# Optimization experiments

Measured on AMD Instinct MI355X. Metric: run time of the kernel, lower is better.

## Reference

```python
import jax, jax.numpy as jnp
import numpy as np

D_MODEL = 1024
N_HEADS = 16
D_HEAD = D_MODEL // N_HEADS
BATCH = 2
SEQ = 2048


def setup_inputs() -> dict:
    key = jax.random.key(0)
    ks = jax.random.split(key, 16)
    s = 0.02
    d = D_MODEL
    return {
        "x": jax.random.normal(ks[0], (BATCH, SEQ, d), jnp.float32),
        "Wq": jax.random.normal(ks[1], (d, d), jnp.float32) * s,
        "bq": jnp.zeros((d,), jnp.float32),
        "Wk": jax.random.normal(ks[2], (d, d), jnp.float32) * s,
        "bk": jnp.zeros((d,), jnp.float32),
        "Wv": jax.random.normal(ks[3], (d, d), jnp.float32) * s,
        "bv": jnp.zeros((d,), jnp.float32),
        "Wo": jax.random.normal(ks[4], (d, d), jnp.float32) * s,
        "bo": jnp.zeros((d,), jnp.float32),
        "Wt": jax.random.normal(ks[5], (d, 1), jnp.float32) * s,
        "bt": jnp.zeros((1,), jnp.float32),
        "Wg": jax.random.normal(ks[6], (d, d), jnp.float32) * s,
        "bg": jnp.zeros((d,), jnp.float32),
    }


def _evolved_attention(x, Wq, bq, Wk, bk, Wv, bv, Wo, bo, Wt, bt, Wg, bg):
    B, S, D = x.shape
    H, dh = N_HEADS, D_HEAD

    def heads(y):  # [B,S,D] -> [B,H,S,dh]
        return y.reshape(B, S, H, dh).transpose(0, 2, 1, 3)

    q = heads(x @ Wq + bq)
    k = heads(x @ Wk + bk)
    v = heads(x @ Wv + bv)

    # cosine similarity (F.normalize with eps=1e-12)
    qn = q / jnp.maximum(jnp.linalg.norm(q, axis=-1, keepdims=True), 1e-12)
    kn = k / jnp.maximum(jnp.linalg.norm(k, axis=-1, keepdims=True), 1e-12)
    scores = jnp.einsum("bhqd,bhkd->bhqk", qn, kn)

    # adaptive temperature: sigmoid(temp_proj(mean_s x)) + 0.5, shape [B,1]
    temp = jax.nn.sigmoid(x.mean(axis=1) @ Wt + bt) + 0.5  # [B,1]
    scores = scores / temp[:, None, None, :]  # broadcast [B,1,1,1]

    # sparsemax-style: softmax over top-k (k = S//4), scattered back
    kk = max(1, S // 4)
    vals, idx = jax.lax.top_k(scores, kk)          # [B,H,S,kk]
    w = jax.nn.softmax(vals, axis=-1)
    rows = jnp.arange(B * H * S)[:, None]
    attn = (
        jnp.zeros((B * H * S, S), scores.dtype)
        .at[rows, idx.reshape(-1, kk)]
        .set(w.reshape(-1, kk))
        .reshape(B, H, S, S)
    )

    out = jnp.einsum("bhqk,bhkd->bhqd", attn, v)
    out = out.transpose(0, 2, 1, 3).reshape(B, S, D)
    out = out @ Wo + bo

    # highway gating
    gate = jax.nn.sigmoid(x @ Wg + bg)
    return gate * out + (1.0 - gate) * x


def reference(x, Wq, bq, Wk, bk, Wv, bv, Wo, bo, Wt, bt, Wg, bg):
    return _evolved_attention(x, Wq, bq, Wk, bk, Wv, bv, Wo, bo, Wt, bt, Wg, bg)
```

## Files before the change

### kernel.cpp

```cpp
#include <hip/hip_runtime.h>

typedef unsigned short u16;
typedef __attribute__((ext_vector_type(4))) float f32x4;
typedef __attribute__((ext_vector_type(8))) short bf16x8;
typedef __attribute__((ext_vector_type(4))) int i32x4;

#define BB 2
#define SS 2048
#define DD 1024
#define HH 16
#define DH 64
#define KK 512

#define OFF_SCAL  ((size_t)0)
#define OFF_WT    ((size_t)256)
#define OFF_XB    (OFF_WT + (size_t)5*1024*1024*2)
#define OFF_AO    OFF_XB
#define OFF_QH    (OFF_XB + (size_t)4096*1024*2)
#define OFF_QN    (OFF_QH + (size_t)4096*4096*2)
#define OFF_KN    (OFF_QN + (size_t)4096*1024*2)
#define OFF_VT    (OFF_KN + (size_t)4096*1024*2)

__device__ __forceinline__ float b2f(u16 u) { return __uint_as_float(((unsigned)u) << 16); }
__device__ __forceinline__ u16 f2b(float f) {
    unsigned u = __float_as_uint(f);
    return (u16)((u + 0x7fffu + ((u >> 16) & 1u)) >> 16);
}

__global__ __launch_bounds__(256) void convert_x(const float* x, u16* xb) {
    int i = (blockIdx.x * 256 + threadIdx.x) * 4;
    float4 v = *(const float4*)(x + i);
    u16 r0 = f2b(v.x), r1 = f2b(v.y), r2 = f2b(v.z), r3 = f2b(v.w);
    xb[i] = r0; xb[i + 1] = r1; xb[i + 2] = r2; xb[i + 3] = r3;
}

__global__ __launch_bounds__(256) void transpose_w(
        const float* Wq, const float* Wk, const float* Wv, const float* Wg, const float* Wo,
        u16* WT) {
    int z = blockIdx.z;
    const float* src = (z == 0) ? Wq : (z == 1) ? Wk : (z == 2) ? Wv : (z == 3) ? Wg : Wo;
    u16* dst = WT + (size_t)z * 1024 * 1024;
    __shared__ float tile[64][65];
    int n0 = blockIdx.x * 64, k0 = blockIdx.y * 64;
    int rbase = threadIdx.x >> 6, c = threadIdx.x & 63;
#pragma unroll
    for (int i = 0; i < 16; i++) {
        int r = i * 4 + rbase;
        tile[r][c] = src[(size_t)(k0 + r) * 1024 + n0 + c];
    }
    __syncthreads();
#pragma unroll
    for (int i = 0; i < 16; i++) {
        int r = i * 4 + rbase;
        dst[(size_t)(n0 + r) * 1024 + k0 + c] = f2b(tile[c][r]);
    }
}

__global__ __launch_bounds__(256) void temp_partial(const float* x, const float* Wt,
                                                    float* accbuf) {
    int b = blockIdx.x >> 5, ch = blockIdx.x & 31;
    float a = 0.f;
    for (int si = 0; si < 64; si++) {
        int s = ch * 64 + si;
        const float* xr = x + ((size_t)(b * SS + s)) * DD;
#pragma unroll
        for (int k = 0; k < 4; k++) {
            int c = threadIdx.x + k * 256;
            a += xr[c] * Wt[c];
        }
    }
    for (int o = 32; o; o >>= 1) a += __shfl_xor(a, o);
    __shared__ float red[4];
    if ((threadIdx.x & 63) == 0) red[threadIdx.x >> 6] = a;
    __syncthreads();
    if (threadIdx.x == 0) atomicAdd(&accbuf[b], red[0] + red[1] + red[2] + red[3]);
}

__global__ void temp_final(const float* accbuf, const float* bt, float* itemp) {
    int t = threadIdx.x;
    if (t < BB) {
        float v = accbuf[t] / (float)SS + bt[0];
        float tmp = 1.f / (1.f + __expf(-v)) + 0.5f;
        itemp[t] = 1.f / tmp;
    }
}

__global__ __launch_bounds__(256) void gemm_qkvg(
        const u16* X, const u16* WT,
        const float* bq, const float* bk, const float* bv, const float* bg, u16* Qh) {
    __shared__ u16 la[64 * 40];
    __shared__ u16 lb[64 * 40];
    int tid = threadIdx.x, wid = tid >> 6, lane = tid & 63;
    int m0 = blockIdx.x * 64, n0 = blockIdx.y * 64;
    int quad = lane >> 4, ml = lane & 15;
    f32x4 acc[4];
#pragma unroll
    for (int i = 0; i < 4; i++) acc[i] = (f32x4){0.f, 0.f, 0.f, 0.f};

    int sr = tid >> 2, sg = tid & 3;
    for (int k0 = 0; k0 < 1024; k0 += 32) {
        __syncthreads();
        *(i32x4*)&la[sr * 40 + sg * 8] = *(const i32x4*)&X[(size_t)(m0 + sr) * 1024 + k0 + sg * 8];
        *(i32x4*)&lb[sr * 40 + sg * 8] = *(const i32x4*)&WT[(size_t)(n0 + sr) * 1024 + k0 + sg * 8];
        __syncthreads();
        bf16x8 a = *(const bf16x8*)&la[(wid * 16 + ml) * 40 + quad * 8];
#pragma unroll
        for (int nt = 0; nt < 4; nt++) {
            bf16x8 bfr = *(const bf16x8*)&lb[(nt * 16 + ml) * 40 + quad * 8];
            acc[nt] = __builtin_amdgcn_mfma_f32_16x16x32_bf16(a, bfr, acc[nt], 0, 0, 0);
        }
    }
#pragma unroll
    for (int nt = 0; nt < 4; nt++) {
        int col = n0 + nt * 16 + ml;
        int mat = col >> 10, bc = col & 1023;
        const float* bp = (mat == 0) ? bq : (mat == 1) ? bk : (mat == 2) ? bv : bg;
        float bias = bp[bc];
#pragma unroll
        for (int r = 0; r < 4; r++) {
            int row = m0 + wid * 16 + quad * 4 + r;
            Qh[(size_t)row * 4096 + col] = f2b(acc[nt][r] + bias);
        }
    }
}

__global__ __launch_bounds__(256) void norm_repack(const u16* Qh, u16* qn, u16* kn, u16* vt) {
    int wid = threadIdx.x >> 6, lane = threadIdx.x & 63;
    int idx = blockIdx.x * 4 + wid;
    int token = idx >> 4, h = idx & 15;
    int b = token >> 11, s = token & 2047;
    int bh = b * HH + h;
    const u16* rowp = Qh + (size_t)token * 4096 + h * 64;
    float q = b2f(rowp[lane]);
    float k = b2f(rowp[1024 + lane]);
    u16 v = rowp[2048 + lane];
    float sq = q * q, sk = k * k;
    for (int o = 32; o; o >>= 1) { sq += __shfl_xor(sq, o); sk += __shfl_xor(sk, o); }
    float qd = fmaxf(sqrtf(sq), 1e-12f), kd = fmaxf(sqrtf(sk), 1e-12f);
    qn[((size_t)bh * SS + s) * DH + lane] = f2b(q / qd);
    kn[((size_t)bh * SS + s) * DH + lane] = f2b(k / kd);
    vt[((size_t)bh * DH + lane) * SS + s] = v;
}

#define EST 2088

__global__ __launch_bounds__(1024, 8) void attn_kernel(
        const u16* qn, const u16* kn, const u16* vt, const float* itemp, u16* ao) {
    __shared__ __align__(16) u16 e16[16 * EST];
    __shared__ float pvp[3][16][66];
    __shared__ float zrow_s[16];

    int tid = threadIdx.x, wid = tid >> 6, lane = tid & 63;
    int quad = lane >> 4, nl = lane & 15;
    int bh = blockIdx.x >> 7, qt = blockIdx.x & 127;
    int b = bh >> 4, h = bh & 15;
    const u16* qbase = qn + ((size_t)bh * SS + qt * 16) * DH;
    const u16* kbase = kn + (size_t)bh * SS * DH;
    const u16* vbase = vt + (size_t)bh * DH * SS;
    float it = itemp[b];

    bf16x8 aq0 = *(const bf16x8*)(qbase + nl * DH + quad * 8);
    bf16x8 aq1 = *(const bf16x8*)(qbase + nl * DH + 32 + quad * 8);

#pragma unroll 4
    for (int c = 0; c < 8; c++) {
        int j = c * 256 + wid * 16 + nl;
        const u16* kr = kbase + (size_t)j * DH;
        bf16x8 b0 = *(const bf16x8*)(kr + quad * 8);
        bf16x8 b1 = *(const bf16x8*)(kr + 32 + quad * 8);
        f32x4 acc = (f32x4){0.f, 0.f, 0.f, 0.f};
        acc = __builtin_amdgcn_mfma_f32_16x16x32_bf16(aq0, b0, acc, 0, 0, 0);
        acc = __builtin_amdgcn_mfma_f32_16x16x32_bf16(aq1, b1, acc, 0, 0, 0);
#pragma unroll
        for (int r = 0; r < 4; r++) e16[(quad * 4 + r) * EST + j] = f2b(acc[r] * it);
    }
    __syncthreads();

    {
        int row = wid;
        int key[32];
#pragma unroll
        for (int c = 0; c < 32; c++) {
            int raw = (int)e16[row * EST + c * 64 + lane];
            key[c] = (raw & 0x8000) ? (raw ^ 0xFFFF) : (raw | 0x8000);
        }
        int P = 0;
        for (int bit = 15; bit >= 0; bit--) {
            int cand = P | (1 << bit);
            int cnt = 0;
#pragma unroll
            for (int c = 0; c < 32; c++)
                cnt += (int)__popcll(__ballot(key[c] >= cand));
            if (cnt >= KK) P = cand;
        }
        float z = 0.f;
#pragma unroll
        for (int c = 0; c < 32; c++) {
            float e = 0.f;
            if (key[c] >= P) {
                int raw = (key[c] & 0x8000) ? (key[c] ^ 0x8000) : (key[c] ^ 0xFFFF);
                e = __expf(b2f((u16)raw));
            }
            z += e;
            e16[row * EST + c * 64 + lane] = f2b(e);
        }
#pragma unroll
        for (int o = 32; o; o >>= 1) z += __shfl_xor(z, o);
        if (lane == 0) zrow_s[row] = z;
    }
    __syncthreads();

    f32x4 accp = (f32x4){0.f, 0.f, 0.f, 0.f};
    int kq = wid >> 2, g = wid & 3;
    int dh = g * 16 + nl;
    const u16* vrow = vbase + (size_t)dh * SS;
#pragma unroll 4
    for (int c = 0; c < 8; c++) {
        int j0 = kq * 512 + c * 64;
#pragma unroll
        for (int ks = 0; ks < 2; ks++) {
            bf16x8 a = *(const bf16x8*)&e16[nl * EST + j0 + ks * 32 + quad * 8];
            bf16x8 bfr = *(const bf16x8*)(vrow + j0 + ks * 32 + quad * 8);
            accp = __builtin_amdgcn_mfma_f32_16x16x32_bf16(a, bfr, accp, 0, 0, 0);
        }
    }
    if (kq) {
#pragma unroll
        for (int r = 0; r < 4; r++) pvp[kq - 1][quad * 4 + r][dh] = accp[r];
    }
    __syncthreads();
    if (kq == 0) {
#pragma unroll
        for (int r = 0; r < 4; r++) {
            int q = quad * 4 + r;
            float val = (accp[r] + pvp[0][q][dh] + pvp[1][q][dh] + pvp[2][q][dh]) / zrow_s[q];
            size_t row = (size_t)(b * SS + qt * 16 + q);
            ao[row * DD + h * 64 + dh] = f2b(val);
        }
    }
}

__global__ __launch_bounds__(256) void gemm_out(
        const u16* AO, const u16* WTo, const float* bo,
        const u16* Qh, const float* x, float* out) {
    __shared__ u16 la[64 * 40];
    __shared__ u16 lb[64 * 40];
    int tid = threadIdx.x, wid = tid >> 6, lane = tid & 63;
    int m0 = blockIdx.x * 64, n0 = blockIdx.y * 64;
    int quad = lane >> 4, ml = lane & 15;
    f32x4 acc[4];
#pragma unroll
    for (int i = 0; i < 4; i++) acc[i] = (f32x4){0.f, 0.f, 0.f, 0.f};

    int sr = tid >> 2, sg = tid & 3;
    for (int k0 = 0; k0 < 1024; k0 += 32) {
        __syncthreads();
        *(i32x4*)&la[sr * 40 + sg * 8] = *(const i32x4*)&AO[(size_t)(m0 + sr) * 1024 + k0 + sg * 8];
        *(i32x4*)&lb[sr * 40 + sg * 8] = *(const i32x4*)&WTo[(size_t)(n0 + sr) * 1024 + k0 + sg * 8];
        __syncthreads();
        bf16x8 a = *(const bf16x8*)&la[(wid * 16 + ml) * 40 + quad * 8];
#pragma unroll
        for (int nt = 0; nt < 4; nt++) {
            bf16x8 bfr = *(const bf16x8*)&lb[(nt * 16 + ml) * 40 + quad * 8];
            acc[nt] = __builtin_amdgcn_mfma_f32_16x16x32_bf16(a, bfr, acc[nt], 0, 0, 0);
        }
    }
#pragma unroll
    for (int nt = 0; nt < 4; nt++) {
        int col = n0 + nt * 16 + ml;
        float bias = bo[col];
#pragma unroll
        for (int r = 0; r < 4; r++) {
            int row = m0 + wid * 16 + quad * 4 + r;
            float g = b2f(Qh[(size_t)row * 4096 + 3072 + col]);
            float gate = 1.f / (1.f + __expf(-g));
            float xv = x[(size_t)row * 1024 + col];
            float o = acc[nt][r] + bias;
            out[(size_t)row * 1024 + col] = gate * o + (1.f - gate) * xv;
        }
    }
}

extern "C" void kernel_launch(void* const* d_in, const int* in_sizes, int n_in,
                              void* d_out, int out_size, void* d_ws, size_t ws_size,
                              hipStream_t stream) {
    const float* x  = (const float*)d_in[0];
    const float* Wq = (const float*)d_in[1];
    const float* bq = (const float*)d_in[2];
    const float* Wk = (const float*)d_in[3];
    const float* bk = (const float*)d_in[4];
    const float* Wv = (const float*)d_in[5];
    const float* bv = (const float*)d_in[6];
    const float* Wo = (const float*)d_in[7];
    const float* bo = (const float*)d_in[8];
    const float* Wt = (const float*)d_in[9];
    const float* bt = (const float*)d_in[10];
    const float* Wg = (const float*)d_in[11];
    const float* bg = (const float*)d_in[12];

    char* w = (char*)d_ws;
    float* accbuf = (float*)(w + OFF_SCAL);
    float* itemp  = accbuf + 2;
    u16*   WT     = (u16*)(w + OFF_WT);
    u16*   xb     = (u16*)(w + OFF_XB);
    u16*   ao     = (u16*)(w + OFF_AO);
    u16*   Qh     = (u16*)(w + OFF_QH);
    u16*   qn     = (u16*)(w + OFF_QN);
    u16*   kn     = (u16*)(w + OFF_KN);
    u16*   vt     = (u16*)(w + OFF_VT);

    hipMemsetAsync(accbuf, 0, 2 * sizeof(float), stream);

    convert_x<<<4096, 256, 0, stream>>>(x, xb);
    transpose_w<<<dim3(16, 16, 5), 256, 0, stream>>>(Wq, Wk, Wv, Wg, Wo, WT);
    temp_partial<<<64, 256, 0, stream>>>(x, Wt, accbuf);
    temp_final<<<1, 64, 0, stream>>>(accbuf, bt, itemp);
    gemm_qkvg<<<dim3(64, 64), 256, 0, stream>>>(xb, WT, bq, bk, bv, bg, Qh);
    norm_repack<<<16384, 256, 0, stream>>>(Qh, qn, kn, vt);
    attn_kernel<<<4096, 1024, 0, stream>>>(qn, kn, vt, itemp, ao);
    gemm_out<<<dim3(64, 16), 256, 0, stream>>>(ao, WT + (size_t)4 * 1024 * 1024, bo, Qh, x,
                                               (float*)d_out);
}
```

Baseline: 548.1 us.

## Enlarge GEMM tiles with direct-to-LDS loads and vectorize top-k threshold search

Result: faster. 510.6 us (-6.8%).

```diff
diff --git a/kernel.cpp b/kernel.cpp
--- a/kernel.cpp
+++ b/kernel.cpp
@@ -25,6 +25,12 @@
 __device__ __forceinline__ u16 f2b(float f) {
     unsigned u = __float_as_uint(f);
     return (u16)((u + 0x7fffu + ((u >> 16) & 1u)) >> 16);
+}
+
+__device__ __forceinline__ void gload16(const u16* g, u16* l) {
+    __builtin_amdgcn_global_load_lds(
+        (__attribute__((address_space(1))) void*)g,
+        (__attribute__((address_space(3))) void*)l, 16, 0, 0);
 }
 
 __global__ __launch_bounds__(256) void convert_x(const float* x, u16* xb) {
@@ -88,40 +94,64 @@
 __global__ __launch_bounds__(256) void gemm_qkvg(
         const u16* X, const u16* WT,
         const float* bq, const float* bk, const float* bv, const float* bg, u16* Qh) {
-    __shared__ u16 la[64 * 40];
-    __shared__ u16 lb[64 * 40];
+    __shared__ __align__(16) u16 la[128 * 32];
+    __shared__ __align__(16) u16 lb[128 * 32];
     int tid = threadIdx.x, wid = tid >> 6, lane = tid & 63;
-    int m0 = blockIdx.x * 64, n0 = blockIdx.y * 64;
     int quad = lane >> 4, ml = lane & 15;
-    f32x4 acc[4];
-#pragma unroll
-    for (int i = 0; i < 4; i++) acc[i] = (f32x4){0.f, 0.f, 0.f, 0.f};
-
-    int sr = tid >> 2, sg = tid & 3;
+    int m0 = blockIdx.x * 128, n0 = blockIdx.y * 128;
+    int wr = wid >> 1, wc = wid & 1;
+
+    f32x4 acc[4][4];
+#pragma unroll
+    for (int i = 0; i < 4; i++)
+#pragma unroll
+        for (int j = 0; j < 4; j++) acc[i][j] = (f32x4){0.f, 0.f, 0.f, 0.f};
+
+    int t0 = wid * 2, t1 = t0 + 1;
+    int r0 = lane >> 2, kp = lane & 3;
+    const u16* ga0 = X + (size_t)(m0 + t0 * 16 + r0) * 1024 + kp * 8;
+    const u16* ga1 = X + (size_t)(m0 + t1 * 16 + r0) * 1024 + kp * 8;
+    const u16* gb0 = WT + (size_t)(n0 + t0 * 16 + r0) * 1024 + kp * 8;
+    const u16* gb1 = WT + (size_t)(n0 + t1 * 16 + r0) * 1024 + kp * 8;
+    u16* la0 = la + t0 * 512; u16* la1 = la + t1 * 512;
+    u16* lb0 = lb + t0 * 512; u16* lb1 = lb + t1 * 512;
+
     for (int k0 = 0; k0 < 1024; k0 += 32) {
+        gload16(ga0 + k0, la0);
+        gload16(ga1 + k0, la1);
+        gload16(gb0 + k0, lb0);
+        gload16(gb1 + k0, lb1);
         __syncthreads();
-        *(i32x4*)&la[sr * 40 + sg * 8] = *(const i32x4*)&X[(size_t)(m0 + sr) * 1024 + k0 + sg * 8];
-        *(i32x4*)&lb[sr * 40 + sg * 8] = *(const i32x4*)&WT[(size_t)(n0 + sr) * 1024 + k0 + sg * 8];
+        bf16x8 af[4], bfr[4];
+#pragma unroll
+        for (int mi = 0; mi < 4; mi++)
+            af[mi] = *(const bf16x8*)&la[(wr * 64 + mi * 16 + ml) * 32 + quad * 8];
+#pragma unroll
+        for (int ni = 0; ni < 4; ni++)
+            bfr[ni] = *(const bf16x8*)&lb[(wc * 64 + ni * 16 + ml) * 32 + quad * 8];
+#pragma unroll
+        for (int mi = 0; mi < 4; mi++)
+#pragma unroll
+            for (int ni = 0; ni < 4; ni++)
+                acc[mi][ni] = __builtin_amdgcn_mfma_f32_16x16x32_bf16(af[mi], bfr[ni],
+                                                                      acc[mi][ni], 0, 0, 0);
         __syncthreads();
-        bf16x8 a = *(const bf16x8*)&la[(wid * 16 + ml) * 40 + quad * 8];
-#pragma unroll
-        for (int nt = 0; nt < 4; nt++) {
-            bf16x8 bfr = *(const bf16x8*)&lb[(nt * 16 + ml) * 40 + quad * 8];
-            acc[nt] = __builtin_amdgcn_mfma_f32_16x16x32_bf16(a, bfr, acc[nt], 0, 0, 0);
-        }
-    }
-#pragma unroll
-    for (int nt = 0; nt < 4; nt++) {
-        int col = n0 + nt * 16 + ml;
-        int mat = col >> 10, bc = col & 1023;
-        const float* bp = (mat == 0) ? bq : (mat == 1) ? bk : (mat == 2) ? bv : bg;
-        float bias = bp[bc];
-#pragma unroll
-        for (int r = 0; r < 4; r++) {
-            int row = m0 + wid * 16 + quad * 4 + r;
-            Qh[(size_t)row * 4096 + col] = f2b(acc[nt][r] + bias);
-        }
-    }
+    }
+
+#pragma unroll
+    for (int mi = 0; mi < 4; mi++)
+#pragma unroll
+        for (int ni = 0; ni < 4; ni++) {
+            int col = n0 + wc * 64 + ni * 16 + ml;
+            int mat = col >> 10, bc = col & 1023;
+            const float* bp = (mat == 0) ? bq : (mat == 1) ? bk : (mat == 2) ? bv : bg;
+            float bias = bp[bc];
+#pragma unroll
+            for (int r = 0; r < 4; r++) {
+                int row = m0 + wr * 64 + mi * 16 + quad * 4 + r;
+                Qh[(size_t)row * 4096 + col] = f2b(acc[mi][ni][r] + bias);
+            }
+        }
 }
 
 __global__ __launch_bounds__(256) void norm_repack(const u16* Qh, u16* qn, u16* kn, u16* vt) {
@@ -178,31 +208,53 @@
 
     {
         int row = wid;
-        int key[32];
-#pragma unroll
-        for (int c = 0; c < 32; c++) {
-            int raw = (int)e16[row * EST + c * 64 + lane];
-            key[c] = (raw & 0x8000) ? (raw ^ 0xFFFF) : (raw | 0x8000);
-        }
+        u16* rp = &e16[row * EST];
+        int kk[32];
+#pragma unroll
+        for (int i = 0; i < 4; i++) {
+            i32x4 kv = *(const i32x4*)(rp + i * 512 + lane * 8);
+#pragma unroll
+            for (int j = 0; j < 4; j++) {
+                int r2 = kv[j];
+                int t = ((r2 >> 15) & 0x00010001) * 0x7FFF;
+                int key2 = r2 ^ 0x80008000 ^ t;
+                kk[i * 8 + j * 2]     = key2 & 0xFFFF;
+                kk[i * 8 + j * 2 + 1] = ((unsigned)key2) >> 16;
+            }
+        }
+#pragma unroll
+        for (int c = 0; c < 32; c++) asm volatile("" : "+v"(kk[c]));
+
         int P = 0;
         for (int bit = 15; bit >= 0; bit--) {
             int cand = P | (1 << bit);
             int cnt = 0;
 #pragma unroll
             for (int c = 0; c < 32; c++)
-                cnt += (int)__popcll(__ballot(key[c] >= cand));
+                cnt += (int)__popcll(__ballot(kk[c] >= cand));
             if (cnt >= KK) P = cand;
-        }
+            if (cnt == KK) break;
+        }
+
         float z = 0.f;
 #pragma unroll
-        for (int c = 0; c < 32; c++) {
-            float e = 0.f;
-            if (key[c] >= P) {
-                int raw = (key[c] & 0x8000) ? (key[c] ^ 0x8000) : (key[c] ^ 0xFFFF);
-                e = __expf(b2f((u16)raw));
+        for (int i = 0; i < 4; i++) {
+            i32x4 ev;
+#pragma unroll
+            for (int j = 0; j < 4; j++) {
+                int k0i = kk[i * 8 + j * 2], k1i = kk[i * 8 + j * 2 + 1];
+                unsigned r0 = (unsigned)k0i ^ ((k0i & 0x8000) ? 0x8000u : 0xFFFFu);
+                unsigned r1 = (unsigned)k1i ^ ((k1i & 0x8000) ? 0x8000u : 0xFFFFu);
+                float f0 = __uint_as_float(r0 << 16);
+                float f1 = __uint_as_float(r1 << 16);
+                float e0 = (k0i >= P) ? __expf(f0) : 0.f;
+                float e1 = (k1i >= P) ? __expf(f1) : 0.f;
+                z += e0 + e1;
+                int pk;
+                asm("v_cvt_pk_bf16_f32 %0, %1, %2" : "=v"(pk) : "v"(e0), "v"(e1));
+                ev[j] = pk;
             }
-            z += e;
-            e16[row * EST + c * 64 + lane] = f2b(e);
+            *(i32x4*)(rp + i * 512 + lane * 8) = ev;
         }
 #pragma unroll
         for (int o = 32; o; o >>= 1) z += __shfl_xor(z, o);
@@ -243,42 +295,66 @@
 __global__ __launch_bounds__(256) void gemm_out(
         const u16* AO, const u16* WTo, const float* bo,
         const u16* Qh, const float* x, float* out) {
-    __shared__ u16 la[64 * 40];
-    __shared__ u16 lb[64 * 40];
+    __shared__ __align__(16) u16 la[128 * 32];
+    __shared__ __align__(16) u16 lb[128 * 32];
     int tid = threadIdx.x, wid = tid >> 6, lane = tid & 63;
-    int m0 = blockIdx.x * 64, n0 = blockIdx.y * 64;
     int quad = lane >> 4, ml = lane & 15;
-    f32x4 acc[4];
-#pragma unroll
-    for (int i = 0; i < 4; i++) acc[i] = (f32x4){0.f, 0.f, 0.f, 0.f};
-
-    int sr = tid >> 2, sg = tid & 3;
+    int m0 = blockIdx.x * 128, n0 = blockIdx.y * 128;
+    int wr = wid >> 1, wc = wid & 1;
+
+    f32x4 acc[4][4];
+#pragma unroll
+    for (int i = 0; i < 4; i++)
+#pragma unroll
+        for (int j = 0; j < 4; j++) acc[i][j] = (f32x4){0.f, 0.f, 0.f, 0.f};
+
+    int t0 = wid * 2, t1 = t0 + 1;
+    int r0 = lane >> 2, kp = lane & 3;
+    const u16* ga0 = AO + (size_t)(m0 + t0 * 16 + r0) * 1024 + kp * 8;
+    const u16* ga1 = AO + (size_t)(m0 + t1 * 16 + r0) * 1024 + kp * 8;
+    const u16* gb0 = WTo + (size_t)(n0 + t0 * 16 + r0) * 1024 + kp * 8;
+    const u16* gb1 = WTo + (size_t)(n0 + t1 * 16 + r0) * 1024 + kp * 8;
+    u16* la0 = la + t0 * 512; u16* la1 = la + t1 * 512;
+    u16* lb0 = lb + t0 * 512; u16* lb1 = lb + t1 * 512;
+
     for (int k0 = 0; k0 < 1024; k0 += 32) {
+        gload16(ga0 + k0, la0);
+        gload16(ga1 + k0, la1);
+        gload16(gb0 + k0, lb0);
+        gload16(gb1 + k0, lb1);
         __syncthreads();
-        *(i32x4*)&la[sr * 40 + sg * 8] = *(const i32x4*)&AO[(size_t)(m0 + sr) * 1024 + k0 + sg * 8];
-        *(i32x4*)&lb[sr * 40 + sg * 8] = *(const i32x4*)&WTo[(size_t)(n0 + sr) * 1024 + k0 + sg * 8];
+        bf16x8 af[4], bfr[4];
+#pragma unroll
+        for (int mi = 0; mi < 4; mi++)
+            af[mi] = *(const bf16x8*)&la[(wr * 64 + mi * 16 + ml) * 32 + quad * 8];
+#pragma unroll
+        for (int ni = 0; ni < 4; ni++)
+            bfr[ni] = *(const bf16x8*)&lb[(wc * 64 + ni * 16 + ml) * 32 + quad * 8];
+#pragma unroll
+        for (int mi = 0; mi < 4; mi++)
+#pragma unroll
+            for (int ni = 0; ni < 4; ni++)
+                acc[mi][ni] = __builtin_amdgcn_mfma_f32_16x16x32_bf16(af[mi], bfr[ni],
+                                                                      acc[mi][ni], 0, 0, 0);
         __syncthreads();
-        bf16x8 a = *(const bf16x8*)&la[(wid * 16 + ml) * 40 + quad * 8];
-#pragma unroll
-        for (int nt = 0; nt < 4; nt++) {
-            bf16x8 bfr = *(const bf16x8*)&lb[(nt * 16 + ml) * 40 + quad * 8];
-            acc[nt] = __builtin_amdgcn_mfma_f32_16x16x32_bf16(a, bfr, acc[nt], 0, 0, 0);
-        }
-    }
-#pragma unroll
-    for (int nt = 0; nt < 4; nt++) {
-        int col = n0 + nt * 16 + ml;
-        float bias = bo[col];
-#pragma unroll
-        for (int r = 0; r < 4; r++) {
-            int row = m0 + wid * 16 + quad * 4 + r;
-            float g = b2f(Qh[(size_t)row * 4096 + 3072 + col]);
-            float gate = 1.f / (1.f + __expf(-g));
-            float xv = x[(size_t)row * 1024 + col];
-            float o = acc[nt][r] + bias;
-            out[(size_t)row * 1024 + col] = gate * o + (1.f - gate) * xv;
-        }
-    }
+    }
+
+#pragma unroll
+    for (int mi = 0; mi < 4; mi++)
+#pragma unroll
+        for (int ni = 0; ni < 4; ni++) {
+            int col = n0 + wc * 64 + ni * 16 + ml;
+            float bias = bo[col];
+#pragma unroll
+            for (int r = 0; r < 4; r++) {
+                int row = m0 + wr * 64 + mi * 16 + quad * 4 + r;
+                float gv = b2f(Qh[(size_t)row * 4096 + 3072 + col]);
+                float gate = 1.f / (1.f + __expf(-gv));
+                float xv = x[(size_t)row * 1024 + col];
+                float o = acc[mi][ni][r] + bias;
+                out[(size_t)row * 1024 + col] = gate * o + (1.f - gate) * xv;
+            }
+        }
 }
 
 extern "C" void kernel_launch(void* const* d_in, const int* in_sizes, int n_in,
@@ -315,9 +391,9 @@
     transpose_w<<<dim3(16, 16, 5), 256, 0, stream>>>(Wq, Wk, Wv, Wg, Wo, WT);
     temp_partial<<<64, 256, 0, stream>>>(x, Wt, accbuf);
     temp_final<<<1, 64, 0, stream>>>(accbuf, bt, itemp);
-    gemm_qkvg<<<dim3(64, 64), 256, 0, stream>>>(xb, WT, bq, bk, bv, bg, Qh);
+    gemm_qkvg<<<dim3(32, 32), 256, 0, stream>>>(xb, WT, bq, bk, bv, bg, Qh);
     norm_repack<<<16384, 256, 0, stream>>>(Qh, qn, kn, vt);
     attn_kernel<<<4096, 1024, 0, stream>>>(qn, kn, vt, itemp, ao);
-    gemm_out<<<dim3(64, 16), 256, 0, stream>>>(ao, WT + (size_t)4 * 1024 * 1024, bo, Qh, x,
-                                               (float*)d_out);
-}
+    gemm_out<<<dim3(32, 8), 256, 0, stream>>>(ao, WT + (size_t)4 * 1024 * 1024, bo, Qh, x,
+                                              (float*)d_out);
+}
```
